# Kernel optimization log

Hardware: AMD Instinct MI355X
Metric: run time of the kernel (lower is better)

Reference implementation:

```python
import jax, jax.numpy as jnp
import numpy as np

N_NODES = 50000
N_EDGES = 640000
D_IN = 128
D_H1 = 128
D_H2 = 128
N_CLASSES = 64


def setup_inputs() -> dict:
    key = jax.random.key(0)
    ks = jax.random.split(key, 8)
    x = jax.random.normal(ks[0], (N_NODES, D_IN), dtype=jnp.float32)
    edge_index = jax.random.randint(ks[1], (2, N_EDGES), 0, N_NODES, dtype=jnp.int64)
    s1 = 1.0 / np.sqrt(D_IN)
    s2 = 1.0 / np.sqrt(D_H1)
    s3 = 1.0 / np.sqrt(D_H2)
    W1 = jax.random.uniform(ks[2], (D_IN, D_H1), jnp.float32, -s1, s1)
    b1 = jnp.zeros((D_H1,), jnp.float32)
    W2 = jax.random.uniform(ks[3], (D_H1, D_H2), jnp.float32, -s2, s2)
    b2 = jnp.zeros((D_H2,), jnp.float32)
    Wl = jax.random.uniform(ks[4], (D_H2, N_CLASSES), jnp.float32, -s3, s3)
    bl = jax.random.uniform(ks[5], (N_CLASSES,), jnp.float32, -s3, s3)
    return {"x": x, "edge_index": edge_index, "W1": W1, "b1": b1,
            "W2": W2, "b2": b2, "Wl": Wl, "bl": bl}


def _gcn_norm(edge_index, num_nodes):
    # PyG GCNConv: add self-loops, symmetric normalization D^-1/2 (A+I) D^-1/2
    loop = jnp.arange(num_nodes, dtype=edge_index.dtype)
    src = jnp.concatenate([edge_index[0], loop])
    dst = jnp.concatenate([edge_index[1], loop])
    deg = jax.ops.segment_sum(jnp.ones_like(dst, dtype=jnp.float32), dst,
                              num_segments=num_nodes)
    dinv = jnp.where(deg > 0, jax.lax.rsqrt(deg), 0.0)
    norm = dinv[src] * dinv[dst]  # [E+N]
    return src, dst, norm


def _gcn_conv(h, src, dst, norm, W, b, num_nodes):
    h = h @ W                       # transform first (smaller gather when D_out small)
    msg = h[src] * norm[:, None]    # gather + per-edge scale  [E+N, D_out]
    agg = jax.ops.segment_sum(msg, dst, num_segments=num_nodes)  # scatter-add
    return agg + b


def reference(x, edge_index, W1, b1, W2, b2, Wl, bl):
    n = x.shape[0]
    src, dst, norm = _gcn_norm(edge_index, n)
    h = jax.nn.relu(_gcn_conv(x, src, dst, norm, W1, b1, n))
    # dropout is identity in eval mode
    h = jax.nn.relu(_gcn_conv(h, src, dst, norm, W2, b2, n))
    return h @ Wl + bl
```

## Files before the change

### kernel.cpp

```cpp
#include <hip/hip_runtime.h>


typedef __attribute__((ext_vector_type(8))) __bf16 bf16x8;
typedef __attribute__((ext_vector_type(8))) short short8;
typedef __attribute__((ext_vector_type(4))) float f32x4;

__device__ inline float bf_lo(unsigned u) { return __uint_as_float(u << 16); }
__device__ inline float bf_hi(unsigned u) { return __uint_as_float(u & 0xffff0000u); }
__device__ inline unsigned short f2bf(float v) {
  return __builtin_bit_cast(unsigned short, (__bf16)v);
}

__global__ void k_count(const int* __restrict__ dst, int E,
                        int* __restrict__ cnt, int* __restrict__ rank) {
  int i = blockIdx.x * blockDim.x + threadIdx.x;
  if (i < E) rank[i] = atomicAdd(&cnt[dst[i]], 1);
}

__global__ void k_scan1_prepW(const int* __restrict__ cnt, int n, int* __restrict__ partial,
                              int nb,
                              const float* __restrict__ W1, const float* __restrict__ W2,
                              const float* __restrict__ Wl,
                              unsigned short* __restrict__ b1h, unsigned short* __restrict__ b1l,
                              unsigned short* __restrict__ b2h, unsigned short* __restrict__ b2l,
                              unsigned short* __restrict__ blh, unsigned short* __restrict__ bll) {
  if ((int)blockIdx.x < nb) {
    __shared__ int s[256];
    int i = blockIdx.x * 256 + threadIdx.x;
    s[threadIdx.x] = (i < n) ? cnt[i] : 0;
    __syncthreads();
    for (int off = 128; off > 0; off >>= 1) {
      if (threadIdx.x < off) s[threadIdx.x] += s[threadIdx.x + off];
      __syncthreads();
    }
    if (threadIdx.x == 0) partial[blockIdx.x] = s[0];
  } else {
    int idx = ((int)blockIdx.x - nb) * 256 + threadIdx.x;
    const float* W;
    unsigned short *bh, *bl_;
    int N, local;
    if (idx < 16384)      { W = W1; bh = b1h; bl_ = b1l; N = 128; local = idx; }
    else if (idx < 32768) { W = W2; bh = b2h; bl_ = b2l; N = 128; local = idx - 16384; }
    else if (idx < 40960) { W = Wl; bh = blh; bl_ = bll; N = 64;  local = idx - 32768; }
    else return;
    int nn = local >> 7, k = local & 127;
    float v = W[(size_t)k * N + nn];
    __bf16 h = (__bf16)v;
    bh[local] = __builtin_bit_cast(unsigned short, h);
    bl_[local] = f2bf(v - (float)h);
  }
}

__global__ void k_scan3(const int* __restrict__ cnt, const int* __restrict__ partial,
                        int nb, int n, int* __restrict__ row_off,
                        float* __restrict__ dinv) {
  __shared__ int s[256];
  __shared__ int base_s;
  int t = threadIdx.x;
  s[t] = (t < nb && t < (int)blockIdx.x) ? partial[t] : 0;
  __syncthreads();
  for (int off = 128; off > 0; off >>= 1) {
    if (t < off) s[t] += s[t + off];
    __syncthreads();
  }
  if (t == 0) base_s = s[0];
  __syncthreads();
  int base = base_s;
  __syncthreads();

  int i = blockIdx.x * 256 + t;
  int v = (i < n) ? cnt[i] : 0;
  s[t] = v;
  __syncthreads();
  for (int off = 1; off < 256; off <<= 1) {
    int u = (t >= off) ? s[t - off] : 0;
    __syncthreads();
    s[t] += u;
    __syncthreads();
  }
  int incl = s[t];
  int excl = incl - v;
  if (i < n) {
    row_off[i] = base + excl;
    dinv[i] = rsqrtf((float)(v + 1));
    if (i == n - 1) row_off[n] = base + incl;
  }
}

__global__ void k_place(const int* __restrict__ src, const int* __restrict__ dst,
                        const int* __restrict__ rank, const int* __restrict__ row_off,
                        int E, int* __restrict__ edges) {
  int e = blockIdx.x * blockDim.x + threadIdx.x;
  if (e < E) {
    int d = dst[e];
    int pos = row_off[d] + rank[e];
    __builtin_nontemporal_store(src[e], &edges[pos]);
  }
}

template <int NT, bool A32, bool BIAS, bool OUT_BF16, bool SCALE>
__global__ __launch_bounds__(256) void gemm3(
    const void* __restrict__ Ahi_, const unsigned short* __restrict__ Alo,
    const unsigned short* __restrict__ Bhi, const unsigned short* __restrict__ Blo,
    const float* __restrict__ bias, const float* __restrict__ dinv,
    void* __restrict__ Cout, int M) {
  constexpr int K = 128;
  constexpr int NCOL = NT * 16;
  __shared__ alignas(16) unsigned short lbh[NCOL * K];
  __shared__ alignas(16) unsigned short lbl[NCOL * K];
  int t = threadIdx.x;
  int lane = t & 63, wave = t >> 6;
  int lm = lane & 15, lk = lane >> 4;
  int m_base = blockIdx.x * 128 + wave * 32;
  const short8 zero8 = {0, 0, 0, 0, 0, 0, 0, 0};

  if (SCALE && blockIdx.x == 0 && t < 64) {
    *(unsigned*)&((unsigned short*)Cout)[(size_t)M * NCOL + t * 2] = 0u;
  }

  bf16x8 ah[2][4], al[2][4];
  if (A32) {
    const float* Af = (const float*)Ahi_;
    float4 ra[2][4][2];
#pragma unroll
    for (int mt = 0; mt < 2; ++mt) {
      int row = m_base + mt * 16 + lm;
#pragma unroll
      for (int ks = 0; ks < 4; ++ks) {
        if (row < M) {
          ra[mt][ks][0] = *(const float4*)&Af[(size_t)row * K + ks * 32 + lk * 8];
          ra[mt][ks][1] = *(const float4*)&Af[(size_t)row * K + ks * 32 + lk * 8 + 4];
        } else {
          ra[mt][ks][0] = make_float4(0.f, 0.f, 0.f, 0.f);
          ra[mt][ks][1] = make_float4(0.f, 0.f, 0.f, 0.f);
        }
      }
    }
#pragma unroll
    for (int mt = 0; mt < 2; ++mt)
#pragma unroll
      for (int ks = 0; ks < 4; ++ks) {
        float av[8] = {ra[mt][ks][0].x, ra[mt][ks][0].y, ra[mt][ks][0].z, ra[mt][ks][0].w,
                       ra[mt][ks][1].x, ra[mt][ks][1].y, ra[mt][ks][1].z, ra[mt][ks][1].w};
#pragma unroll
        for (int j = 0; j < 8; ++j) {
          __bf16 h = (__bf16)av[j];
          ah[mt][ks][j] = h;
          al[mt][ks][j] = (__bf16)(av[j] - (float)h);
        }
      }
  } else {
    const unsigned short* Ahi = (const unsigned short*)Ahi_;
#pragma unroll
    for (int mt = 0; mt < 2; ++mt) {
      int row = m_base + mt * 16 + lm;
#pragma unroll
      for (int ks = 0; ks < 4; ++ks) {
        if (row < M) {
          ah[mt][ks] = *(const bf16x8*)&Ahi[(size_t)row * K + ks * 32 + lk * 8];
          al[mt][ks] = *(const bf16x8*)&Alo[(size_t)row * K + ks * 32 + lk * 8];
        } else {
          ah[mt][ks] = __builtin_bit_cast(bf16x8, zero8);
          al[mt][ks] = __builtin_bit_cast(bf16x8, zero8);
        }
      }
    }
  }

  for (int c = t; c < NCOL * 16; c += 256) {
    int r = c >> 4, q = c & 15;
    int sq = q ^ (r & 15);
    *(short8*)&lbh[r * K + sq * 8] = *(const short8*)&Bhi[r * K + q * 8];
    *(short8*)&lbl[r * K + sq * 8] = *(const short8*)&Blo[r * K + q * 8];
  }
  __syncthreads();

  f32x4 acc[2][NT] = {};
#pragma unroll
  for (int ks = 0; ks < 4; ++ks) {
    int chunk = ks * 4 + lk;
    bf16x8 bh[NT], bl[NT];
#pragma unroll
    for (int nt = 0; nt < NT; ++nt) {
      int r = nt * 16 + lm;
      int sq = chunk ^ lm;
      bh[nt] = *(const bf16x8*)&lbh[r * K + sq * 8];
      bl[nt] = *(const bf16x8*)&lbl[r * K + sq * 8];
    }
#pragma unroll
    for (int mt = 0; mt < 2; ++mt)
#pragma unroll
      for (int nt = 0; nt < NT; ++nt) {
        acc[mt][nt] = __builtin_amdgcn_mfma_f32_16x16x32_bf16(ah[mt][ks], bh[nt], acc[mt][nt], 0, 0, 0);
        acc[mt][nt] = __builtin_amdgcn_mfma_f32_16x16x32_bf16(ah[mt][ks], bl[nt], acc[mt][nt], 0, 0, 0);
        acc[mt][nt] = __builtin_amdgcn_mfma_f32_16x16x32_bf16(al[mt][ks], bh[nt], acc[mt][nt], 0, 0, 0);
      }
  }

#pragma unroll
  for (int mt = 0; mt < 2; ++mt) {
#pragma unroll
    for (int r = 0; r < 4; ++r) {
      int row = m_base + mt * 16 + lk * 4 + r;
      if (row < M) {
        float dr = SCALE ? dinv[row] : 1.f;
#pragma unroll
        for (int nt = 0; nt < NT; ++nt) {
          int col = nt * 16 + lm;
          float v = acc[mt][nt][r];
          if (SCALE) v *= dr;
          if (BIAS) v += bias[col];
          if (OUT_BF16)
            ((unsigned short*)Cout)[(size_t)row * NCOL + col] = f2bf(v);
          else
            __builtin_nontemporal_store(v, &((float*)Cout)[(size_t)row * NCOL + col]);
        }
      }
    }
  }
}

__global__ __launch_bounds__(256) void k_agg(const unsigned short* __restrict__ t,
                      const int* __restrict__ row_off,
                      const int* __restrict__ edges,
                      const float* __restrict__ dinv, const float* __restrict__ bias,
                      unsigned short* __restrict__ ghi, unsigned short* __restrict__ glo,
                      int n) {
  int wave = threadIdx.x >> 6;
  int lane = threadIdx.x & 63;
  int g = lane >> 4;
  int fl = lane & 15;
  int node = blockIdx.x * 4 + wave;
  if (node >= n) return;
  int2 ro = *(const int2*)&row_off[node];
  int e0 = ro.x, e1 = ro.y;
  int last = e1 - 1;

  float acc[8] = {};
  for (int base = e0; base < e1; base += 8) {
    int i0 = base + g, i1 = base + 4 + g;
    int s0 = edges[i0 < e1 ? i0 : last];
    int s1 = edges[i1 < e1 ? i1 : last];
    s0 = i0 < e1 ? s0 : n;
    s1 = i1 < e1 ? s1 : n;
    uint4 u0 = *(const uint4*)&t[(size_t)s0 * 128 + fl * 8];
    uint4 u1 = *(const uint4*)&t[(size_t)s1 * 128 + fl * 8];
    acc[0] += bf_lo(u0.x) + bf_lo(u1.x);
    acc[1] += bf_hi(u0.x) + bf_hi(u1.x);
    acc[2] += bf_lo(u0.y) + bf_lo(u1.y);
    acc[3] += bf_hi(u0.y) + bf_hi(u1.y);
    acc[4] += bf_lo(u0.z) + bf_lo(u1.z);
    acc[5] += bf_hi(u0.z) + bf_hi(u1.z);
    acc[6] += bf_lo(u0.w) + bf_lo(u1.w);
    acc[7] += bf_hi(u0.w) + bf_hi(u1.w);
  }
#pragma unroll
  for (int j = 0; j < 8; ++j) {
    acc[j] += __shfl_xor(acc[j], 16);
    acc[j] += __shfl_xor(acc[j], 32);
  }
  if (g == 0) {
    float di = dinv[node];
    uint4 sv = *(const uint4*)&t[(size_t)node * 128 + fl * 8];
    acc[0] += bf_lo(sv.x); acc[1] += bf_hi(sv.x);
    acc[2] += bf_lo(sv.y); acc[3] += bf_hi(sv.y);
    acc[4] += bf_lo(sv.z); acc[5] += bf_hi(sv.z);
    acc[6] += bf_lo(sv.w); acc[7] += bf_hi(sv.w);
    float4 bb0 = *(const float4*)&bias[fl * 8];
    float4 bb1 = *(const float4*)&bias[fl * 8 + 4];
    float bb[8] = {bb0.x, bb0.y, bb0.z, bb0.w, bb1.x, bb1.y, bb1.z, bb1.w};
    short8 ho, lo_;
#pragma unroll
    for (int j = 0; j < 8; ++j) {
      float s = fmaxf(acc[j] * di + bb[j], 0.f);
      __bf16 h = (__bf16)s;
      ho[j] = __builtin_bit_cast(short, h);
      lo_[j] = (short)f2bf(s - (float)h);
    }
    *(short8*)&ghi[(size_t)node * 128 + fl * 8] = ho;
    *(short8*)&glo[(size_t)node * 128 + fl * 8] = lo_;
  }
}

extern "C" void kernel_launch(void* const* d_in, const int* in_sizes, int n_in,
                              void* d_out, int out_size, void* d_ws, size_t ws_size,
                              hipStream_t stream) {
  const float* x  = (const float*)d_in[0];
  const int*   ei = (const int*)d_in[1];
  const float* W1 = (const float*)d_in[2];
  const float* b1 = (const float*)d_in[3];
  const float* W2 = (const float*)d_in[4];
  const float* b2 = (const float*)d_in[5];
  const float* Wl = (const float*)d_in[6];
  const float* bl = (const float*)d_in[7];
  float* out = (float*)d_out;

  const int D = 128;
  int N = in_sizes[0] / D;
  int E = in_sizes[1] / 2;
  const int* src = ei;
  const int* dst = ei + E;

  uintptr_t ws = (uintptr_t)d_ws;
  auto take = [&](size_t bytes) {
    uintptr_t p = ws;
    ws += (bytes + 15) & ~(size_t)15;
    return p;
  };
  unsigned short* t_bf = (unsigned short*)take(((size_t)N + 1) * D * 2);
  unsigned short* xh   = (unsigned short*)take((size_t)N * D * 2);
  unsigned short* xl   = (unsigned short*)take((size_t)N * D * 2);
  int*   edges   = (int*)take((size_t)E * 4);
  int*   rank    = (int*)take((size_t)E * 4);
  int*   cnt     = (int*)take((size_t)N * sizeof(int));
  int*   row_off = (int*)take(((size_t)N + 1) * sizeof(int));
  float* dinv    = (float*)take((size_t)N * sizeof(float));
  int*   partial = (int*)take(256 * sizeof(int));
  unsigned short* b1h = (unsigned short*)take(128 * 128 * 2);
  unsigned short* b1l = (unsigned short*)take(128 * 128 * 2);
  unsigned short* b2h = (unsigned short*)take(128 * 128 * 2);
  unsigned short* b2l = (unsigned short*)take(128 * 128 * 2);
  unsigned short* blh = (unsigned short*)take(128 * 64 * 2);
  unsigned short* bll = (unsigned short*)take(128 * 64 * 2);

  int nb_n = (N + 255) / 256;
  int nb_e = (E + 255) / 256;

  hipMemsetAsync(cnt, 0, (size_t)N * sizeof(int), stream);
  k_count<<<nb_e, 256, 0, stream>>>(dst, E, cnt, rank);
  k_scan1_prepW<<<nb_n + 160, 256, 0, stream>>>(cnt, N, partial, nb_n,
                                                W1, W2, Wl, b1h, b1l, b2h, b2l, blh, bll);
  k_scan3<<<nb_n, 256, 0, stream>>>(cnt, partial, nb_n, N, row_off, dinv);
  k_place<<<nb_e, 256, 0, stream>>>(src, dst, rank, row_off, E, edges);

  int gemm_blocks = (N + 127) / 128;
  int agg_blocks = (N + 3) / 4;

  gemm3<8, true, false, true, true><<<gemm_blocks, 256, 0, stream>>>(
      x, nullptr, b1h, b1l, nullptr, dinv, t_bf, N);
  k_agg<<<agg_blocks, 256, 0, stream>>>(t_bf, row_off, edges, dinv, b1, xh, xl, N);
  gemm3<8, false, false, true, true><<<gemm_blocks, 256, 0, stream>>>(
      xh, xl, b2h, b2l, nullptr, dinv, t_bf, N);
  k_agg<<<agg_blocks, 256, 0, stream>>>(t_bf, row_off, edges, dinv, b2, xh, xl, N);
  gemm3<4, false, true, false, false><<<gemm_blocks, 256, 0, stream>>>(
      xh, xl, blh, bll, bl, nullptr, out, N);
}
```

Measured before the change: 234.9 us.

## Compress edge indices to 16-bit, vectorize GEMM epilogue, widen aggregation unroll

The CSR edge list is now stored as 16-bit source indices, which halves index traffic in the placement and aggregation kernels. This relies on the node count (plus the padding index) fitting under 65536. The GEMM swaps its MFMA operands so each lane writes four contiguous outputs as one vector store. It also reads the low-part weights straight from global memory instead of staging them in LDS, which frees shared memory. The aggregation kernel gathers 16 edges per iteration instead of 8 and issues its self-row, bias and dinv loads before the loop, adding more loads in flight per wave.

Measured after the change: 240.4 us. +2.4%, slower.

```diff
diff --git a/kernel.cpp b/kernel.cpp
--- a/kernel.cpp
+++ b/kernel.cpp
@@ -89,12 +89,12 @@
 
 __global__ void k_place(const int* __restrict__ src, const int* __restrict__ dst,
                         const int* __restrict__ rank, const int* __restrict__ row_off,
-                        int E, int* __restrict__ edges) {
+                        int E, unsigned short* __restrict__ edges) {
   int e = blockIdx.x * blockDim.x + threadIdx.x;
   if (e < E) {
     int d = dst[e];
     int pos = row_off[d] + rank[e];
-    __builtin_nontemporal_store(src[e], &edges[pos]);
+    __builtin_nontemporal_store((unsigned short)src[e], &edges[pos]);
   }
 }
 
@@ -107,7 +107,6 @@
   constexpr int K = 128;
   constexpr int NCOL = NT * 16;
   __shared__ alignas(16) unsigned short lbh[NCOL * K];
-  __shared__ alignas(16) unsigned short lbl[NCOL * K];
   int t = threadIdx.x;
   int lane = t & 63, wave = t >> 6;
   int lm = lane & 15, lk = lane >> 4;
@@ -171,7 +170,6 @@
     int r = c >> 4, q = c & 15;
     int sq = q ^ (r & 15);
     *(short8*)&lbh[r * K + sq * 8] = *(const short8*)&Bhi[r * K + q * 8];
-    *(short8*)&lbl[r * K + sq * 8] = *(const short8*)&Blo[r * K + q * 8];
   }
   __syncthreads();
 
@@ -183,37 +181,42 @@
 #pragma unroll
     for (int nt = 0; nt < NT; ++nt) {
       int r = nt * 16 + lm;
-      int sq = chunk ^ lm;
-      bh[nt] = *(const bf16x8*)&lbh[r * K + sq * 8];
-      bl[nt] = *(const bf16x8*)&lbl[r * K + sq * 8];
+      bh[nt] = *(const bf16x8*)&lbh[r * K + (chunk ^ lm) * 8];
+      bl[nt] = *(const bf16x8*)&Blo[(size_t)r * K + chunk * 8];
     }
 #pragma unroll
     for (int mt = 0; mt < 2; ++mt)
 #pragma unroll
       for (int nt = 0; nt < NT; ++nt) {
-        acc[mt][nt] = __builtin_amdgcn_mfma_f32_16x16x32_bf16(ah[mt][ks], bh[nt], acc[mt][nt], 0, 0, 0);
-        acc[mt][nt] = __builtin_amdgcn_mfma_f32_16x16x32_bf16(ah[mt][ks], bl[nt], acc[mt][nt], 0, 0, 0);
-        acc[mt][nt] = __builtin_amdgcn_mfma_f32_16x16x32_bf16(al[mt][ks], bh[nt], acc[mt][nt], 0, 0, 0);
+        acc[mt][nt] = __builtin_amdgcn_mfma_f32_16x16x32_bf16(bh[nt], ah[mt][ks], acc[mt][nt], 0, 0, 0);
+        acc[mt][nt] = __builtin_amdgcn_mfma_f32_16x16x32_bf16(bl[nt], ah[mt][ks], acc[mt][nt], 0, 0, 0);
+        acc[mt][nt] = __builtin_amdgcn_mfma_f32_16x16x32_bf16(bh[nt], al[mt][ks], acc[mt][nt], 0, 0, 0);
       }
   }
 
 #pragma unroll
   for (int mt = 0; mt < 2; ++mt) {
-#pragma unroll
-    for (int r = 0; r < 4; ++r) {
-      int row = m_base + mt * 16 + lk * 4 + r;
-      if (row < M) {
-        float dr = SCALE ? dinv[row] : 1.f;
-#pragma unroll
-        for (int nt = 0; nt < NT; ++nt) {
-          int col = nt * 16 + lm;
-          float v = acc[mt][nt][r];
-          if (SCALE) v *= dr;
-          if (BIAS) v += bias[col];
-          if (OUT_BF16)
-            ((unsigned short*)Cout)[(size_t)row * NCOL + col] = f2bf(v);
-          else
-            __builtin_nontemporal_store(v, &((float*)Cout)[(size_t)row * NCOL + col]);
+    int row = m_base + mt * 16 + lm;
+    if (row < M) {
+      float dr = SCALE ? dinv[row] : 1.f;
+#pragma unroll
+      for (int nt = 0; nt < NT; ++nt) {
+        int col0 = nt * 16 + lk * 4;
+        float v0 = acc[mt][nt][0], v1 = acc[mt][nt][1];
+        float v2 = acc[mt][nt][2], v3 = acc[mt][nt][3];
+        if (SCALE) { v0 *= dr; v1 *= dr; v2 *= dr; v3 *= dr; }
+        if (BIAS) {
+          float4 bb = *(const float4*)&bias[col0];
+          v0 += bb.x; v1 += bb.y; v2 += bb.z; v3 += bb.w;
+        }
+        if (OUT_BF16) {
+          unsigned p0 = (unsigned)f2bf(v0) | ((unsigned)f2bf(v1) << 16);
+          unsigned p1 = (unsigned)f2bf(v2) | ((unsigned)f2bf(v3) << 16);
+          uint2 pk = make_uint2(p0, p1);
+          *(uint2*)&((unsigned short*)Cout)[(size_t)row * NCOL + col0] = pk;
+        } else {
+          float4 pk = make_float4(v0, v1, v2, v3);
+          *(float4*)&((float*)Cout)[(size_t)row * NCOL + col0] = pk;
         }
       }
     }
@@ -222,7 +225,7 @@
 
 __global__ __launch_bounds__(256) void k_agg(const unsigned short* __restrict__ t,
                       const int* __restrict__ row_off,
-                      const int* __restrict__ edges,
+                      const unsigned short* __restrict__ edges,
                       const float* __restrict__ dinv, const float* __restrict__ bias,
                       unsigned short* __restrict__ ghi, unsigned short* __restrict__ glo,
                       int n) {
@@ -236,23 +239,34 @@
   int e0 = ro.x, e1 = ro.y;
   int last = e1 - 1;
 
+  float di = dinv[node];
+  uint4 sv = *(const uint4*)&t[(size_t)node * 128 + fl * 8];
+  float4 bb0 = *(const float4*)&bias[fl * 8];
+  float4 bb1 = *(const float4*)&bias[fl * 8 + 4];
+
   float acc[8] = {};
-  for (int base = e0; base < e1; base += 8) {
-    int i0 = base + g, i1 = base + 4 + g;
+  for (int base = e0; base < e1; base += 16) {
+    int i0 = base + g, i1 = i0 + 4, i2 = i0 + 8, i3 = i0 + 12;
     int s0 = edges[i0 < e1 ? i0 : last];
     int s1 = edges[i1 < e1 ? i1 : last];
+    int s2 = edges[i2 < e1 ? i2 : last];
+    int s3 = edges[i3 < e1 ? i3 : last];
     s0 = i0 < e1 ? s0 : n;
     s1 = i1 < e1 ? s1 : n;
+    s2 = i2 < e1 ? s2 : n;
+    s3 = i3 < e1 ? s3 : n;
     uint4 u0 = *(const uint4*)&t[(size_t)s0 * 128 + fl * 8];
     uint4 u1 = *(const uint4*)&t[(size_t)s1 * 128 + fl * 8];
-    acc[0] += bf_lo(u0.x) + bf_lo(u1.x);
-    acc[1] += bf_hi(u0.x) + bf_hi(u1.x);
-    acc[2] += bf_lo(u0.y) + bf_lo(u1.y);
-    acc[3] += bf_hi(u0.y) + bf_hi(u1.y);
-    acc[4] += bf_lo(u0.z) + bf_lo(u1.z);
-    acc[5] += bf_hi(u0.z) + bf_hi(u1.z);
-    acc[6] += bf_lo(u0.w) + bf_lo(u1.w);
-    acc[7] += bf_hi(u0.w) + bf_hi(u1.w);
+    uint4 u2 = *(const uint4*)&t[(size_t)s2 * 128 + fl * 8];
+    uint4 u3 = *(const uint4*)&t[(size_t)s3 * 128 + fl * 8];
+    acc[0] += (bf_lo(u0.x) + bf_lo(u1.x)) + (bf_lo(u2.x) + bf_lo(u3.x));
+    acc[1] += (bf_hi(u0.x) + bf_hi(u1.x)) + (bf_hi(u2.x) + bf_hi(u3.x));
+    acc[2] += (bf_lo(u0.y) + bf_lo(u1.y)) + (bf_lo(u2.y) + bf_lo(u3.y));
+    acc[3] += (bf_hi(u0.y) + bf_hi(u1.y)) + (bf_hi(u2.y) + bf_hi(u3.y));
+    acc[4] += (bf_lo(u0.z) + bf_lo(u1.z)) + (bf_lo(u2.z) + bf_lo(u3.z));
+    acc[5] += (bf_hi(u0.z) + bf_hi(u1.z)) + (bf_hi(u2.z) + bf_hi(u3.z));
+    acc[6] += (bf_lo(u0.w) + bf_lo(u1.w)) + (bf_lo(u2.w) + bf_lo(u3.w));
+    acc[7] += (bf_hi(u0.w) + bf_hi(u1.w)) + (bf_hi(u2.w) + bf_hi(u3.w));
   }
 #pragma unroll
   for (int j = 0; j < 8; ++j) {
@@ -260,14 +274,10 @@
     acc[j] += __shfl_xor(acc[j], 32);
   }
   if (g == 0) {
-    float di = dinv[node];
-    uint4 sv = *(const uint4*)&t[(size_t)node * 128 + fl * 8];
     acc[0] += bf_lo(sv.x); acc[1] += bf_hi(sv.x);
     acc[2] += bf_lo(sv.y); acc[3] += bf_hi(sv.y);
     acc[4] += bf_lo(sv.z); acc[5] += bf_hi(sv.z);
     acc[6] += bf_lo(sv.w); acc[7] += bf_hi(sv.w);
-    float4 bb0 = *(const float4*)&bias[fl * 8];
-    float4 bb1 = *(const float4*)&bias[fl * 8 + 4];
     float bb[8] = {bb0.x, bb0.y, bb0.z, bb0.w, bb1.x, bb1.y, bb1.z, bb1.w};
     short8 ho, lo_;
 #pragma unroll
@@ -310,7 +320,7 @@
   unsigned short* t_bf = (unsigned short*)take(((size_t)N + 1) * D * 2);
   unsigned short* xh   = (unsigned short*)take((size_t)N * D * 2);
   unsigned short* xl   = (unsigned short*)take((size_t)N * D * 2);
-  int*   edges   = (int*)take((size_t)E * 4);
+  unsigned short* edges = (unsigned short*)take((size_t)E * 2);
   int*   rank    = (int*)take((size_t)E * 4);
   int*   cnt     = (int*)take((size_t)N * sizeof(int));
   int*   row_off = (int*)take(((size_t)N + 1) * sizeof(int));
```
